# Kernel tuning notes

Measured on AMD Instinct MI355X. Metric: run time of the kernel, lower is better.

Reference implementation:

```python
import jax, jax.numpy as jnp
import numpy as np

L = 0.05  # lx = ly = lz box half-extent

# 8 box corners [8,3]
_CORNERS = jnp.array([[sx * L, sy * L, sz * L]
                      for sx in (-1.0, 1.0) for sy in (-1.0, 1.0) for sz in (-1.0, 1.0)],
                     dtype=jnp.float32)
# match original ordering: [-,-,-],[-,-,+],[-,+,-],... which the comprehension above yields


def _euler_R(pose):
    """pose: [B,6] -> R [B,3,3], t [B,3] (yaw, pitch, roll convention from source)."""
    yaw, pitch, roll = pose[:, 0], pose[:, 1], pose[:, 2]
    cy, sy = jnp.cos(yaw), jnp.sin(yaw)
    cp, sp = jnp.cos(pitch), jnp.sin(pitch)
    cr, sr = jnp.cos(roll), jnp.sin(roll)
    R = jnp.stack([
        jnp.stack([cy * cp, cy * sp * sr - sy * cr, cy * sp * cr + sy * sr], axis=-1),
        jnp.stack([sy * cp, sy * sp * sr + cy * cr, sy * sp * cr - cy * sr], axis=-1),
        jnp.stack([-sp, cp * sr, cp * cr], axis=-1),
    ], axis=-2)  # [B,3,3]
    t = pose[:, 3:]  # [B,3]
    return R, t


def _transform_corners(pose):
    R, t = _euler_R(pose)
    # [B,8,3] = corners @ R^T + t
    return jnp.einsum('bij,nj->bni', R, _CORNERS) + t[:, None, :]


def setup_inputs() -> dict:
    key = jax.random.key(0)
    k1, k2, k3, k4 = jax.random.split(key, 4)
    B, C = 1048576, 16
    return {
        'pred_pose': jax.random.normal(k1, (B, 6), dtype=jnp.float32),
        'pred_class': jax.random.normal(k2, (B, C), dtype=jnp.float32),
        'target_pose': jax.random.normal(k3, (B, 6), dtype=jnp.float32),
        'target_class': jax.random.normal(k4, (B, C), dtype=jnp.float32),
    }


def reference(pred_pose, pred_class, target_pose, target_class):
    pts_pred = _transform_corners(pred_pose)    # [B,8,3]
    pts_gt = _transform_corners(target_pose)    # [B,8,3]
    # per-sample pose diff: mean over 8 corner L2 norms, then mean over batch
    norms = jnp.linalg.norm(pts_pred - pts_gt, axis=-1)  # [B,8]
    loss_pose = norms.mean(axis=-1).mean()
    class_loss = jnp.mean((pred_class - target_class) ** 2)
    total_loss = loss_pose + class_loss
    return total_loss, loss_pose, class_loss
```

## Files before the change

kernel.cpp:

```cpp
#include <hip/hip_runtime.h>
#include <math.h>

#define CORNER_L 0.05f

constexpr int THREADS = 256;
constexpr int BLOCKS  = 1024;

__device__ __forceinline__ void euler_R(float yaw, float pitch, float roll, float R[9]) {
    float cy, sy, cp, sp, cr, sr;
    __sincosf(yaw,   &sy, &cy);
    __sincosf(pitch, &sp, &cp);
    __sincosf(roll,  &sr, &cr);
    R[0] = cy * cp;
    R[1] = cy * sp * sr - sy * cr;
    R[2] = cy * sp * cr + sy * sr;
    R[3] = sy * cp;
    R[4] = sy * sp * sr + cy * cr;
    R[5] = sy * sp * cr - cy * sr;
    R[6] = -sp;
    R[7] = cp * sr;
    R[8] = cp * cr;
}

__device__ __forceinline__ float pose_elem(
    float py, float pp_, float pr, float ptx, float pty, float ptz,
    float ty, float tp_, float tr, float ttx, float tty, float ttz)
{
    float Rp[9], Rg[9];
    euler_R(py, pp_, pr, Rp);
    euler_R(ty, tp_, tr, Rg);
    float dtx = ptx - ttx;
    float dty = pty - tty;
    float dtz = ptz - ttz;

    float a0 = CORNER_L * (Rp[0] - Rg[0]), a1 = CORNER_L * (Rp[1] - Rg[1]), a2 = CORNER_L * (Rp[2] - Rg[2]);
    float b0 = CORNER_L * (Rp[3] - Rg[3]), b1 = CORNER_L * (Rp[4] - Rg[4]), b2 = CORNER_L * (Rp[5] - Rg[5]);
    float c0 = CORNER_L * (Rp[6] - Rg[6]), c1 = CORNER_L * (Rp[7] - Rg[7]), c2 = CORNER_L * (Rp[8] - Rg[8]);

    float nsum = 0.0f;
    #pragma unroll
    for (int s = 0; s < 8; ++s) {
        float sx = (s & 4) ? 1.0f : -1.0f;
        float sy = (s & 2) ? 1.0f : -1.0f;
        float sz = (s & 1) ? 1.0f : -1.0f;
        float d0 = sx * a0 + sy * a1 + sz * a2 + dtx;
        float d1 = sx * b0 + sy * b1 + sz * b2 + dty;
        float d2 = sx * c0 + sy * c1 + sz * c2 + dtz;
        nsum += sqrtf(d0 * d0 + d1 * d1 + d2 * d2);
    }
    return nsum;
}

__global__ __launch_bounds__(THREADS, 4) void pose_loss_reduce(
    const float4* __restrict__ pp4,
    const float4* __restrict__ pc4,
    const float4* __restrict__ tp4,
    const float4* __restrict__ tc4,
    float* __restrict__ ws, int B)
{
    __shared__ float s_p[3072];
    __shared__ float s_t[3072];

    const int tid = threadIdx.x;
    const int elems_per_blk = B / gridDim.x;
    const int elem_base = blockIdx.x * elems_per_blk;

    float class_acc0 = 0.0f, class_acc1 = 0.0f;
    float pose_acc = 0.0f;

    {
        const int n4 = elems_per_blk * 4;
        const size_t base = (size_t)elem_base * 4;
        #pragma unroll 4
        for (int k = tid; k < n4; k += 2 * THREADS) {
            float4 p0 = pc4[base + k];
            float4 t0 = tc4[base + k];
            float4 p1 = pc4[base + k + THREADS];
            float4 t1 = tc4[base + k + THREADS];
            float dx0 = p0.x - t0.x, dy0 = p0.y - t0.y, dz0 = p0.z - t0.z, dw0 = p0.w - t0.w;
            float dx1 = p1.x - t1.x, dy1 = p1.y - t1.y, dz1 = p1.z - t1.z, dw1 = p1.w - t1.w;
            class_acc0 += dx0 * dx0 + dy0 * dy0 + dz0 * dz0 + dw0 * dw0;
            class_acc1 += dx1 * dx1 + dy1 * dy1 + dz1 * dz1 + dw1 * dw1;
        }
    }
    float class_acc = class_acc0 + class_acc1;

    const int sub_elems = elems_per_blk / 2;
    float4* sp4 = (float4*)s_p;
    float4* st4 = (float4*)s_t;
    for (int sc = 0; sc < 2; ++sc) {
        const int ebase = elem_base + sc * sub_elems;
        const int nf4 = sub_elems * 6 / 4;
        const size_t gbase = (size_t)ebase * 6 / 4;
        #pragma unroll
        for (int k = tid; k < 768; k += THREADS) {
            sp4[k] = pp4[gbase + k];
            st4[k] = tp4[gbase + k];
        }
        __syncthreads();
        {
            float4 A  = sp4[tid * 3 + 0];
            float4 Bv = sp4[tid * 3 + 1];
            float4 Cv = sp4[tid * 3 + 2];
            float4 D  = st4[tid * 3 + 0];
            float4 E  = st4[tid * 3 + 1];
            float4 F  = st4[tid * 3 + 2];
            pose_acc += pose_elem(A.x, A.y, A.z, A.w, Bv.x, Bv.y,
                                  D.x, D.y, D.z, D.w, E.x, E.y);
            pose_acc += pose_elem(Bv.z, Bv.w, Cv.x, Cv.y, Cv.z, Cv.w,
                                  E.z, E.w, F.x, F.y, F.z, F.w);
        }
        __syncthreads();
    }

    #pragma unroll
    for (int off = 32; off > 0; off >>= 1) {
        pose_acc  += __shfl_down(pose_acc,  off);
        class_acc += __shfl_down(class_acc, off);
    }
    __shared__ float r_pose[4], r_class[4];
    const int lane = tid & 63;
    const int wave = tid >> 6;
    if (lane == 0) { r_pose[wave] = pose_acc; r_class[wave] = class_acc; }
    __syncthreads();
    if (tid == 0) {
        ws[blockIdx.x]             = r_pose[0] + r_pose[1] + r_pose[2] + r_pose[3];
        ws[gridDim.x + blockIdx.x] = r_class[0] + r_class[1] + r_class[2] + r_class[3];
    }
}

__global__ __launch_bounds__(THREADS) void pose_loss_finalize(
    const float* __restrict__ ws, float* __restrict__ out,
    int nblocks, float inv_pose, float inv_class)
{
    float p = 0.0f, c = 0.0f;
    for (int k = threadIdx.x; k < nblocks; k += THREADS) {
        p += ws[k];
        c += ws[nblocks + k];
    }
    #pragma unroll
    for (int off = 32; off > 0; off >>= 1) {
        p += __shfl_down(p, off);
        c += __shfl_down(c, off);
    }
    __shared__ float r_p[4], r_c[4];
    const int lane = threadIdx.x & 63;
    const int wave = threadIdx.x >> 6;
    if (lane == 0) { r_p[wave] = p; r_c[wave] = c; }
    __syncthreads();
    if (threadIdx.x == 0) {
        float lp = (r_p[0] + r_p[1] + r_p[2] + r_p[3]) * inv_pose;
        float lc = (r_c[0] + r_c[1] + r_c[2] + r_c[3]) * inv_class;
        out[0] = lp + lc;
        out[1] = lp;
        out[2] = lc;
    }
}

extern "C" void kernel_launch(void* const* d_in, const int* in_sizes, int n_in,
                              void* d_out, int out_size, void* d_ws, size_t ws_size,
                              hipStream_t stream) {
    const float4* pred_pose    = (const float4*)d_in[0];
    const float4* pred_class   = (const float4*)d_in[1];
    const float4* target_pose  = (const float4*)d_in[2];
    const float4* target_class = (const float4*)d_in[3];
    float* out = (float*)d_out;
    float* ws  = (float*)d_ws;

    const int B = in_sizes[0] / 6;

    pose_loss_reduce<<<BLOCKS, THREADS, 0, stream>>>(pred_pose, pred_class,
                                                     target_pose, target_class, ws, B);

    const float inv_pose  = 1.0f / (8.0f  * (float)B);
    const float inv_class = 1.0f / (16.0f * (float)B);
    pose_loss_finalize<<<1, THREADS, 0, stream>>>(ws, out, BLOCKS, inv_pose, inv_class);
}
```

Baseline: 197.6 us.

## Split class and pose work into separate specialized blocks with direct register loads

The grid now holds 1536 blocks, interleaved so that two of every three do the class MSE and one does the pose loss. The shared-memory staging and both __syncthreads barriers are gone from the pose path. Each pose thread now loads six contiguous float4s per array straight into registers. Class blocks issue eight float4 loads per array before computing, to raise memory-level parallelism. Blocks now differ in work type and size, and the pose loads per thread are strided, which can hurt coalescing.

```diff
diff --git a/kernel.cpp b/kernel.cpp
--- a/kernel.cpp
+++ b/kernel.cpp
@@ -3,8 +3,10 @@
 
 #define CORNER_L 0.05f
 
-constexpr int THREADS = 256;
-constexpr int BLOCKS  = 1024;
+constexpr int THREADS      = 256;
+constexpr int CLASS_BLOCKS = 1024;
+constexpr int POSE_BLOCKS  = 512;
+constexpr int TOTAL_BLOCKS = CLASS_BLOCKS + POSE_BLOCKS;
 
 __device__ __forceinline__ void euler_R(float yaw, float pitch, float roll, float R[9]) {
     float cy, sy, cp, sp, cr, sr;
@@ -58,59 +60,57 @@
     const float4* __restrict__ tc4,
     float* __restrict__ ws, int B)
 {
-    __shared__ float s_p[3072];
-    __shared__ float s_t[3072];
+    const int tid = threadIdx.x;
+    const int g   = blockIdx.x;
+    const int q   = g / 3;
+    const int r   = g - q * 3;
 
-    const int tid = threadIdx.x;
-    const int elems_per_blk = B / gridDim.x;
-    const int elem_base = blockIdx.x * elems_per_blk;
+    float pose_acc  = 0.0f;
+    float class_acc = 0.0f;
 
-    float class_acc0 = 0.0f, class_acc1 = 0.0f;
-    float pose_acc = 0.0f;
+    if (r < 2) {
+        const int cb = q * 2 + r;
+        const size_t cbase = (size_t)cb * 4096;
+        float acc0 = 0.f, acc1 = 0.f;
+        #pragma unroll
+        for (int round = 0; round < 2; ++round) {
+            const size_t base = cbase + round * 2048 + tid;
+            float4 p[8], t[8];
+            #pragma unroll
+            for (int j = 0; j < 8; ++j) p[j] = pc4[base + j * 256];
+            #pragma unroll
+            for (int j = 0; j < 8; ++j) t[j] = tc4[base + j * 256];
+            #pragma unroll
+            for (int j = 0; j < 8; ++j) {
+                float dx = p[j].x - t[j].x, dy = p[j].y - t[j].y;
+                float dz = p[j].z - t[j].z, dw = p[j].w - t[j].w;
+                if (j & 1) acc1 += dx * dx + dy * dy + dz * dz + dw * dw;
+                else       acc0 += dx * dx + dy * dy + dz * dz + dw * dw;
+            }
+        }
+        class_acc = acc0 + acc1;
+    } else {
+        const int pb = q;
+        const size_t ebase = (size_t)pb * 2048;
+        #pragma unroll
+        for (int round = 0; round < 2; ++round) {
+            const size_t elem0 = ebase + round * 1024 + tid * 4;
+            const size_t f4 = (elem0 >> 2) * 6;
+            float4 P[6], T[6];
+            #pragma unroll
+            for (int j = 0; j < 6; ++j) P[j] = pp4[f4 + j];
+            #pragma unroll
+            for (int j = 0; j < 6; ++j) T[j] = tp4[f4 + j];
 
-    {
-        const int n4 = elems_per_blk * 4;
-        const size_t base = (size_t)elem_base * 4;
-        #pragma unroll 4
-        for (int k = tid; k < n4; k += 2 * THREADS) {
-            float4 p0 = pc4[base + k];
-            float4 t0 = tc4[base + k];
-            float4 p1 = pc4[base + k + THREADS];
-            float4 t1 = tc4[base + k + THREADS];
-            float dx0 = p0.x - t0.x, dy0 = p0.y - t0.y, dz0 = p0.z - t0.z, dw0 = p0.w - t0.w;
-            float dx1 = p1.x - t1.x, dy1 = p1.y - t1.y, dz1 = p1.z - t1.z, dw1 = p1.w - t1.w;
-            class_acc0 += dx0 * dx0 + dy0 * dy0 + dz0 * dz0 + dw0 * dw0;
-            class_acc1 += dx1 * dx1 + dy1 * dy1 + dz1 * dz1 + dw1 * dw1;
+            pose_acc += pose_elem(P[0].x, P[0].y, P[0].z, P[0].w, P[1].x, P[1].y,
+                                  T[0].x, T[0].y, T[0].z, T[0].w, T[1].x, T[1].y);
+            pose_acc += pose_elem(P[1].z, P[1].w, P[2].x, P[2].y, P[2].z, P[2].w,
+                                  T[1].z, T[1].w, T[2].x, T[2].y, T[2].z, T[2].w);
+            pose_acc += pose_elem(P[3].x, P[3].y, P[3].z, P[3].w, P[4].x, P[4].y,
+                                  T[3].x, T[3].y, T[3].z, T[3].w, T[4].x, T[4].y);
+            pose_acc += pose_elem(P[4].z, P[4].w, P[5].x, P[5].y, P[5].z, P[5].w,
+                                  T[4].z, T[4].w, T[5].x, T[5].y, T[5].z, T[5].w);
         }
-    }
-    float class_acc = class_acc0 + class_acc1;
-
-    const int sub_elems = elems_per_blk / 2;
-    float4* sp4 = (float4*)s_p;
-    float4* st4 = (float4*)s_t;
-    for (int sc = 0; sc < 2; ++sc) {
-        const int ebase = elem_base + sc * sub_elems;
-        const int nf4 = sub_elems * 6 / 4;
-        const size_t gbase = (size_t)ebase * 6 / 4;
-        #pragma unroll
-        for (int k = tid; k < 768; k += THREADS) {
-            sp4[k] = pp4[gbase + k];
-            st4[k] = tp4[gbase + k];
-        }
-        __syncthreads();
-        {
-            float4 A  = sp4[tid * 3 + 0];
-            float4 Bv = sp4[tid * 3 + 1];
-            float4 Cv = sp4[tid * 3 + 2];
-            float4 D  = st4[tid * 3 + 0];
-            float4 E  = st4[tid * 3 + 1];
-            float4 F  = st4[tid * 3 + 2];
-            pose_acc += pose_elem(A.x, A.y, A.z, A.w, Bv.x, Bv.y,
-                                  D.x, D.y, D.z, D.w, E.x, E.y);
-            pose_acc += pose_elem(Bv.z, Bv.w, Cv.x, Cv.y, Cv.z, Cv.w,
-                                  E.z, E.w, F.x, F.y, F.z, F.w);
-        }
-        __syncthreads();
     }
 
     #pragma unroll
@@ -124,8 +124,8 @@
     if (lane == 0) { r_pose[wave] = pose_acc; r_class[wave] = class_acc; }
     __syncthreads();
     if (tid == 0) {
-        ws[blockIdx.x]             = r_pose[0] + r_pose[1] + r_pose[2] + r_pose[3];
-        ws[gridDim.x + blockIdx.x] = r_class[0] + r_class[1] + r_class[2] + r_class[3];
+        ws[2 * g]     = r_pose[0] + r_pose[1] + r_pose[2] + r_pose[3];
+        ws[2 * g + 1] = r_class[0] + r_class[1] + r_class[2] + r_class[3];
     }
 }
 
@@ -135,8 +135,8 @@
 {
     float p = 0.0f, c = 0.0f;
     for (int k = threadIdx.x; k < nblocks; k += THREADS) {
-        p += ws[k];
-        c += ws[nblocks + k];
+        p += ws[2 * k];
+        c += ws[2 * k + 1];
     }
     #pragma unroll
     for (int off = 32; off > 0; off >>= 1) {
@@ -169,10 +169,10 @@
 
     const int B = in_sizes[0] / 6;
 
-    pose_loss_reduce<<<BLOCKS, THREADS, 0, stream>>>(pred_pose, pred_class,
-                                                     target_pose, target_class, ws, B);
+    pose_loss_reduce<<<TOTAL_BLOCKS, THREADS, 0, stream>>>(pred_pose, pred_class,
+                                                           target_pose, target_class, ws, B);
 
     const float inv_pose  = 1.0f / (8.0f  * (float)B);
     const float inv_class = 1.0f / (16.0f * (float)B);
-    pose_loss_finalize<<<1, THREADS, 0, stream>>>(ws, out, BLOCKS, inv_pose, inv_class);
+    pose_loss_finalize<<<1, THREADS, 0, stream>>>(ws, out, TOTAL_BLOCKS, inv_pose, inv_class);
 }
```

Result: faster. 191.5 us (-3.1%).

## Drop LDS staging, use grid-strided global loads and double the grid

Applied to the files above, without the earlier changes.

Pose data is now loaded directly from global memory as three float4 per thread, and the class data uses a grid-strided pattern with four independent loads per iteration, replacing the shared-memory staging and its barriers. The grid is doubled to 2048 blocks so each thread handles a fixed amount of work. Trig uses separate __sinf/__cosf, the rotation math is inlined, and the hardware sqrt builtin replaces sqrtf. The partial-sum workspace is interleaved per block. Together these aim to remove LDS traffic and synchronisation and to raise memory-level parallelism, at the cost of uncoalesced 48-byte strided pose loads per thread and hard-coded assumptions about B.

```diff
diff --git a/kernel.cpp b/kernel.cpp
--- a/kernel.cpp
+++ b/kernel.cpp
@@ -4,38 +4,31 @@
 #define CORNER_L 0.05f
 
 constexpr int THREADS = 256;
-constexpr int BLOCKS  = 1024;
-
-__device__ __forceinline__ void euler_R(float yaw, float pitch, float roll, float R[9]) {
-    float cy, sy, cp, sp, cr, sr;
-    __sincosf(yaw,   &sy, &cy);
-    __sincosf(pitch, &sp, &cp);
-    __sincosf(roll,  &sr, &cr);
-    R[0] = cy * cp;
-    R[1] = cy * sp * sr - sy * cr;
-    R[2] = cy * sp * cr + sy * sr;
-    R[3] = sy * cp;
-    R[4] = sy * sp * sr + cy * cr;
-    R[5] = sy * sp * cr - cy * sr;
-    R[6] = -sp;
-    R[7] = cp * sr;
-    R[8] = cp * cr;
-}
+constexpr int BLOCKS  = 2048;
 
 __device__ __forceinline__ float pose_elem(
     float py, float pp_, float pr, float ptx, float pty, float ptz,
     float ty, float tp_, float tr, float ttx, float tty, float ttz)
 {
-    float Rp[9], Rg[9];
-    euler_R(py, pp_, pr, Rp);
-    euler_R(ty, tp_, tr, Rg);
+    float sy1 = __sinf(py),  cy1 = __cosf(py);
+    float sp1 = __sinf(pp_), cp1 = __cosf(pp_);
+    float sr1 = __sinf(pr),  cr1 = __cosf(pr);
+    float sy2 = __sinf(ty),  cy2 = __cosf(ty);
+    float sp2 = __sinf(tp_), cp2 = __cosf(tp_);
+    float sr2 = __sinf(tr),  cr2 = __cosf(tr);
+
+    float a0 = CORNER_L * (cy1 * cp1 - cy2 * cp2);
+    float a1 = CORNER_L * ((cy1 * sp1 * sr1 - sy1 * cr1) - (cy2 * sp2 * sr2 - sy2 * cr2));
+    float a2 = CORNER_L * ((cy1 * sp1 * cr1 + sy1 * sr1) - (cy2 * sp2 * cr2 + sy2 * sr2));
+    float b0 = CORNER_L * (sy1 * cp1 - sy2 * cp2);
+    float b1 = CORNER_L * ((sy1 * sp1 * sr1 + cy1 * cr1) - (sy2 * sp2 * sr2 + cy2 * cr2));
+    float b2 = CORNER_L * ((sy1 * sp1 * cr1 - cy1 * sr1) - (sy2 * sp2 * cr2 - cy2 * sr2));
+    float c0 = CORNER_L * (sp2 - sp1);
+    float c1 = CORNER_L * (cp1 * sr1 - cp2 * sr2);
+    float c2 = CORNER_L * (cp1 * cr1 - cp2 * cr2);
     float dtx = ptx - ttx;
     float dty = pty - tty;
     float dtz = ptz - ttz;
-
-    float a0 = CORNER_L * (Rp[0] - Rg[0]), a1 = CORNER_L * (Rp[1] - Rg[1]), a2 = CORNER_L * (Rp[2] - Rg[2]);
-    float b0 = CORNER_L * (Rp[3] - Rg[3]), b1 = CORNER_L * (Rp[4] - Rg[4]), b2 = CORNER_L * (Rp[5] - Rg[5]);
-    float c0 = CORNER_L * (Rp[6] - Rg[6]), c1 = CORNER_L * (Rp[7] - Rg[7]), c2 = CORNER_L * (Rp[8] - Rg[8]);
 
     float nsum = 0.0f;
     #pragma unroll
@@ -46,7 +39,7 @@
         float d0 = sx * a0 + sy * a1 + sz * a2 + dtx;
         float d1 = sx * b0 + sy * b1 + sz * b2 + dty;
         float d2 = sx * c0 + sy * c1 + sz * c2 + dtz;
-        nsum += sqrtf(d0 * d0 + d1 * d1 + d2 * d2);
+        nsum += __builtin_amdgcn_sqrtf(d0 * d0 + d1 * d1 + d2 * d2);
     }
     return nsum;
 }
@@ -58,59 +51,46 @@
     const float4* __restrict__ tc4,
     float* __restrict__ ws, int B)
 {
-    __shared__ float s_p[3072];
-    __shared__ float s_t[3072];
+    const int tid  = threadIdx.x;
+    const size_t gtid = (size_t)blockIdx.x * THREADS + tid;
+    const size_t G    = (size_t)BLOCKS * THREADS;
 
-    const int tid = threadIdx.x;
-    const int elems_per_blk = B / gridDim.x;
-    const int elem_base = blockIdx.x * elems_per_blk;
+    float class_acc = 0.0f;
+    {
+        float acc0 = 0.f, acc1 = 0.f, acc2 = 0.f, acc3 = 0.f;
+        #pragma unroll
+        for (int r = 0; r < 2; ++r) {
+            const size_t base = gtid + (size_t)r * 4 * G;
+            float4 p0 = pc4[base];
+            float4 p1 = pc4[base + G];
+            float4 p2 = pc4[base + 2 * G];
+            float4 p3 = pc4[base + 3 * G];
+            float4 t0 = tc4[base];
+            float4 t1 = tc4[base + G];
+            float4 t2 = tc4[base + 2 * G];
+            float4 t3 = tc4[base + 3 * G];
+            float dx, dy, dz, dw;
+            dx = p0.x - t0.x; dy = p0.y - t0.y; dz = p0.z - t0.z; dw = p0.w - t0.w;
+            acc0 += dx * dx + dy * dy + dz * dz + dw * dw;
+            dx = p1.x - t1.x; dy = p1.y - t1.y; dz = p1.z - t1.z; dw = p1.w - t1.w;
+            acc1 += dx * dx + dy * dy + dz * dz + dw * dw;
+            dx = p2.x - t2.x; dy = p2.y - t2.y; dz = p2.z - t2.z; dw = p2.w - t2.w;
+            acc2 += dx * dx + dy * dy + dz * dz + dw * dw;
+            dx = p3.x - t3.x; dy = p3.y - t3.y; dz = p3.z - t3.z; dw = p3.w - t3.w;
+            acc3 += dx * dx + dy * dy + dz * dz + dw * dw;
+        }
+        class_acc = (acc0 + acc1) + (acc2 + acc3);
+    }
 
-    float class_acc0 = 0.0f, class_acc1 = 0.0f;
     float pose_acc = 0.0f;
-
     {
-        const int n4 = elems_per_blk * 4;
-        const size_t base = (size_t)elem_base * 4;
-        #pragma unroll 4
-        for (int k = tid; k < n4; k += 2 * THREADS) {
-            float4 p0 = pc4[base + k];
-            float4 t0 = tc4[base + k];
-            float4 p1 = pc4[base + k + THREADS];
-            float4 t1 = tc4[base + k + THREADS];
-            float dx0 = p0.x - t0.x, dy0 = p0.y - t0.y, dz0 = p0.z - t0.z, dw0 = p0.w - t0.w;
-            float dx1 = p1.x - t1.x, dy1 = p1.y - t1.y, dz1 = p1.z - t1.z, dw1 = p1.w - t1.w;
-            class_acc0 += dx0 * dx0 + dy0 * dy0 + dz0 * dz0 + dw0 * dw0;
-            class_acc1 += dx1 * dx1 + dy1 * dy1 + dz1 * dz1 + dw1 * dw1;
-        }
-    }
-    float class_acc = class_acc0 + class_acc1;
-
-    const int sub_elems = elems_per_blk / 2;
-    float4* sp4 = (float4*)s_p;
-    float4* st4 = (float4*)s_t;
-    for (int sc = 0; sc < 2; ++sc) {
-        const int ebase = elem_base + sc * sub_elems;
-        const int nf4 = sub_elems * 6 / 4;
-        const size_t gbase = (size_t)ebase * 6 / 4;
-        #pragma unroll
-        for (int k = tid; k < 768; k += THREADS) {
-            sp4[k] = pp4[gbase + k];
-            st4[k] = tp4[gbase + k];
-        }
-        __syncthreads();
-        {
-            float4 A  = sp4[tid * 3 + 0];
-            float4 Bv = sp4[tid * 3 + 1];
-            float4 Cv = sp4[tid * 3 + 2];
-            float4 D  = st4[tid * 3 + 0];
-            float4 E  = st4[tid * 3 + 1];
-            float4 F  = st4[tid * 3 + 2];
-            pose_acc += pose_elem(A.x, A.y, A.z, A.w, Bv.x, Bv.y,
-                                  D.x, D.y, D.z, D.w, E.x, E.y);
-            pose_acc += pose_elem(Bv.z, Bv.w, Cv.x, Cv.y, Cv.z, Cv.w,
-                                  E.z, E.w, F.x, F.y, F.z, F.w);
-        }
-        __syncthreads();
+        const size_t f4 = gtid * 3;
+        float4 P0 = pp4[f4], P1 = pp4[f4 + 1], P2 = pp4[f4 + 2];
+        float4 T0 = tp4[f4], T1 = tp4[f4 + 1], T2 = tp4[f4 + 2];
+        pose_acc += pose_elem(P0.x, P0.y, P0.z, P0.w, P1.x, P1.y,
+                              T0.x, T0.y, T0.z, T0.w, T1.x, T1.y);
+        pose_acc += pose_elem(P1.z, P1.w, P2.x, P2.y, P2.z, P2.w,
+                              T1.z, T1.w, T2.x, T2.y, T2.z, T2.w);
     }
 
     #pragma unroll
@@ -124,8 +104,8 @@
     if (lane == 0) { r_pose[wave] = pose_acc; r_class[wave] = class_acc; }
     __syncthreads();
     if (tid == 0) {
-        ws[blockIdx.x]             = r_pose[0] + r_pose[1] + r_pose[2] + r_pose[3];
-        ws[gridDim.x + blockIdx.x] = r_class[0] + r_class[1] + r_class[2] + r_class[3];
+        ws[2 * blockIdx.x]     = r_pose[0] + r_pose[1] + r_pose[2] + r_pose[3];
+        ws[2 * blockIdx.x + 1] = r_class[0] + r_class[1] + r_class[2] + r_class[3];
     }
 }
 
@@ -135,8 +115,8 @@
 {
     float p = 0.0f, c = 0.0f;
     for (int k = threadIdx.x; k < nblocks; k += THREADS) {
-        p += ws[k];
-        c += ws[nblocks + k];
+        p += ws[2 * k];
+        c += ws[2 * k + 1];
     }
     #pragma unroll
     for (int off = 32; off > 0; off >>= 1) {
```

Measured after the change: 189.0 us. 1.05x faster.
